# Kernel tuning notes

Measured on AMD Instinct MI355X. Metric: run time of the kernel, lower is better.

Reference implementation:

```python
import jax, jax.numpy as jnp
import numpy as np

EPS = 1e-5

def _layernorm(h, g, b):
    m = jnp.mean(h, axis=-1, keepdims=True)
    v = jnp.mean((h - m) ** 2, axis=-1, keepdims=True)
    return (h - m) * jax.lax.rsqrt(v + EPS) * g + b

def setup_inputs() -> dict:
    key = jax.random.key(0)
    ks = jax.random.split(key, 12)
    B, C, T = 8, 512, 8192
    TOK, CD = 256, 768
    s = 0.02
    return {
        "x": jax.random.normal(ks[0], (B, C, T), dtype=jnp.float32),
        "context": jax.random.normal(ks[1], (B, TOK, CD), dtype=jnp.float32),
        "context_mask": jax.random.randint(ks[2], (B, TOK), 0, 2).astype(bool),
        "ln_g": jnp.ones((C,), jnp.float32),
        "ln_b": jnp.zeros((C,), jnp.float32),
        "cln_g": jnp.ones((CD,), jnp.float32),
        "cln_b": jnp.zeros((CD,), jnp.float32),
        "Wq": jax.random.normal(ks[3], (C, C), jnp.float32) * s,
        "bq": jnp.zeros((C,), jnp.float32),
        "Wk": jax.random.normal(ks[4], (C, CD), jnp.float32) * s,
        "bk": jnp.zeros((C,), jnp.float32),
        "Wv": jax.random.normal(ks[5], (C, CD), jnp.float32) * s,
        "bv": jnp.zeros((C,), jnp.float32),
    }

def reference(x, context, context_mask, ln_g, ln_b, cln_g, cln_b, Wq, bq, Wk, bk, Wv, bv):
    H = 8
    B, C, T = x.shape
    TOK = context.shape[1]
    D = C // H
    hidden = jnp.swapaxes(x, 1, 2)                     # [B, T, C]
    q = (_layernorm(hidden, ln_g, ln_b) @ Wq.T + bq).reshape(B, T, H, D)
    ctx_n = _layernorm(context, cln_g, cln_b)          # [B, TOK, CD]
    k = (ctx_n @ Wk.T + bk).reshape(B, TOK, H, D)
    v = (ctx_n @ Wv.T + bv).reshape(B, TOK, H, D)
    q = jax.nn.softmax(q, axis=-1)                     # feature map on queries
    m = context_mask[:, :, None, None]
    k = jnp.where(m, k, -jnp.finfo(k.dtype).max)
    v = v * m.astype(v.dtype)
    k = jax.nn.softmax(k, axis=1)                      # softmax over tokens
    attn = jnp.einsum('bnhd,bnhe->bhde', k, v)         # small [B,H,D,D] context matrix
    out = jnp.einsum('bthd,bhde->bthe', q, attn).reshape(B, T, C)
    return x + jnp.swapaxes(out, 1, 2)
```

## Files before the change

kernel.cpp:

```cpp
#include <hip/hip_runtime.h>

#define B_ 8
#define C_ 512
#define T_ 8192
#define TOK_ 256
#define CD_ 768

typedef __attribute__((ext_vector_type(8))) short bf16x8;
typedef __attribute__((ext_vector_type(4))) float f32x4;

__device__ __forceinline__ unsigned short f2bf(float f){
  union { float f; unsigned u; } v; v.f = f;
  return (unsigned short)((v.u + 0x7FFFu + ((v.u >> 16) & 1u)) >> 16);
}

__global__ void pack_wq(const float* __restrict__ Wq, unsigned short* __restrict__ out){
  int slot = blockIdx.x * 256 + threadIdx.x;
  int ln = slot & 63, nt = (slot >> 6) & 31, kk = slot >> 11;
  int n  = nt * 16 + (ln & 15);
  int k0 = kk * 32 + (ln >> 4) * 8;
  bf16x8 v;
  #pragma unroll
  for (int j = 0; j < 8; j++) v[j] = (short)f2bf(Wq[(size_t)n * C_ + k0 + j]);
  *(bf16x8*)&out[(size_t)slot * 8] = v;
}

__global__ void pack_wkv(const float* __restrict__ Wk, const float* __restrict__ Wv,
                         unsigned short* __restrict__ out){
  int slot = blockIdx.x * 256 + threadIdx.x;
  int ln = slot & 63, nt = (slot >> 6) & 7;
  int kkh = slot >> 9;
  int kk = kkh % 24, h = kkh / 24;
  const float* W = (nt < 4) ? Wk : Wv;
  int row = h * 64 + (nt & 3) * 16 + (ln & 15);
  int k0 = kk * 32 + (ln >> 4) * 8;
  bf16x8 v;
  #pragma unroll
  for (int j = 0; j < 8; j++) v[j] = (short)f2bf(W[(size_t)row * CD_ + k0 + j]);
  *(bf16x8*)&out[(size_t)slot * 8] = v;
}

__global__ void ctx_ln(const float* __restrict__ ctx, const float* __restrict__ g,
                       const float* __restrict__ bl, unsigned short* __restrict__ outn){
  int row = blockIdx.x;
  const float* p = ctx + (size_t)row * CD_;
  int tid = threadIdx.x;
  float s1 = 0.f, s2 = 0.f;
  for (int i = tid; i < CD_; i += 256){ float v = p[i]; s1 += v; s2 += v * v; }
  #pragma unroll
  for (int o = 32; o > 0; o >>= 1){ s1 += __shfl_xor(s1, o); s2 += __shfl_xor(s2, o); }
  __shared__ float rs[4][2];
  if ((tid & 63) == 0){ rs[tid >> 6][0] = s1; rs[tid >> 6][1] = s2; }
  __syncthreads();
  s1 = rs[0][0] + rs[1][0] + rs[2][0] + rs[3][0];
  s2 = rs[0][1] + rs[1][1] + rs[2][1] + rs[3][1];
  float m = s1 / (float)CD_;
  float var = s2 / (float)CD_ - m * m;
  float rstd = rsqrtf(var + 1e-5f);
  unsigned short* q = outn + (size_t)row * CD_;
  for (int i = tid; i < CD_; i += 256) q[i] = f2bf((p[i] - m) * rstd * g[i] + bl[i]);
}

__global__ __launch_bounds__(256) void ctx_attn(const unsigned short* __restrict__ ctx_nb,
    const unsigned short* __restrict__ wkv_pk,
    const float* __restrict__ bk, const float* __restrict__ bv,
    const int* __restrict__ mask, unsigned short* __restrict__ apk){
  __shared__ __align__(16) char smem[75776];
  unsigned short* a_st  = (unsigned short*)smem;
  unsigned short* p_lds = (unsigned short*)smem;
  unsigned short* v_lds = (unsigned short*)(smem + 32768);
  unsigned short* al    = (unsigned short*)(smem + 65536);
  float* wred = (float*)(smem + 73728);
  int* msk_l  = (int*)(smem + 74752);

  const int tid = threadIdx.x;
  const int b = blockIdx.x >> 3, h = blockIdx.x & 7;
  msk_l[tid] = mask[b * 256 + tid];

  const unsigned short* cb = ctx_nb + (size_t)b * 256 * CD_;
  const int w = tid >> 6, ln = tid & 63, lc = ln & 15, lk = ln >> 4;

  {
    const bf16x8* src = (const bf16x8*)(cb + (size_t)tid * CD_);
    #pragma unroll
    for (int s = 0; s < 4; s++){
      bf16x8 vv = src[s];
      *(bf16x8*)&a_st[(tid * 32 + s * 8) ^ ((tid & 7) << 3)] = vv;
    }
  }
  const bf16x8* wv_ = (const bf16x8*)wkv_pk;
  const size_t wbase = (size_t)h * 24 * 8 * 64;
  f32x4 acc[4][8];
  #pragma unroll
  for (int i = 0; i < 4; i++)
    #pragma unroll
    for (int j = 0; j < 8; j++) acc[i][j] = (f32x4){0.f,0.f,0.f,0.f};
  bf16x8 bbuf[2][8];
  #pragma unroll
  for (int nt = 0; nt < 8; nt++) bbuf[0][nt] = wv_[wbase + (size_t)(0 * 8 + nt) * 64 + ln];
  __syncthreads();

  for (int kk = 0; kk < 24; kk++){
    int cur = kk & 1;
    if (kk < 23){
      const bf16x8* src = (const bf16x8*)(cb + (size_t)tid * CD_ + (kk + 1) * 32);
      unsigned short* dst = a_st + (cur ^ 1) * 8192;
      #pragma unroll
      for (int s = 0; s < 4; s++){
        bf16x8 vv = src[s];
        *(bf16x8*)&dst[(tid * 32 + s * 8) ^ ((tid & 7) << 3)] = vv;
      }
      #pragma unroll
      for (int nt = 0; nt < 8; nt++)
        bbuf[cur ^ 1][nt] = wv_[wbase + (size_t)((kk + 1) * 8 + nt) * 64 + ln];
    }
    bf16x8 af[4];
    #pragma unroll
    for (int mt = 0; mt < 4; mt++){
      int row = w * 64 + mt * 16 + lc;
      af[mt] = *(const bf16x8*)&a_st[cur * 8192 + ((row * 32 + lk * 8) ^ ((row & 7) << 3))];
    }
    #pragma unroll
    for (int mt = 0; mt < 4; mt++)
      #pragma unroll
      for (int nt = 0; nt < 8; nt++)
        acc[mt][nt] = __builtin_amdgcn_mfma_f32_16x16x32_bf16(af[mt], bbuf[cur][nt], acc[mt][nt], 0, 0, 0);
    __syncthreads();
  }

  float bia[8];
  #pragma unroll
  for (int nt = 0; nt < 8; nt++)
    bia[nt] = (nt < 4) ? bk[h * 64 + nt * 16 + lc] : bv[h * 64 + (nt - 4) * 16 + lc];
  bool mk[4][4];
  #pragma unroll
  for (int mt = 0; mt < 4; mt++)
    #pragma unroll
    for (int r = 0; r < 4; r++)
      mk[mt][r] = msk_l[w * 64 + mt * 16 + lk * 4 + r] != 0;

  float cred[4];
  #pragma unroll
  for (int nt = 0; nt < 4; nt++){
    float mx = -3.402823466e38f;
    #pragma unroll
    for (int mt = 0; mt < 4; mt++)
      #pragma unroll
      for (int r = 0; r < 4; r++)
        if (mk[mt][r]) mx = fmaxf(mx, acc[mt][nt][r] + bia[nt]);
    mx = fmaxf(mx, __shfl_xor(mx, 16));
    mx = fmaxf(mx, __shfl_xor(mx, 32));
    cred[nt] = mx;
  }
  if (lk == 0){
    #pragma unroll
    for (int nt = 0; nt < 4; nt++) wred[w * 64 + nt * 16 + lc] = cred[nt];
  }
  __syncthreads();
  float gmx[4];
  #pragma unroll
  for (int nt = 0; nt < 4; nt++){
    int d = nt * 16 + lc;
    gmx[nt] = fmaxf(fmaxf(wred[d], wred[64 + d]), fmaxf(wred[128 + d], wred[192 + d]));
  }
  __syncthreads();
  #pragma unroll
  for (int nt = 0; nt < 4; nt++){
    float s = 0.f;
    #pragma unroll
    for (int mt = 0; mt < 4; mt++)
      #pragma unroll
      for (int r = 0; r < 4; r++){
        float p = mk[mt][r] ? expf(acc[mt][nt][r] + bia[nt] - gmx[nt]) : 0.f;
        acc[mt][nt][r] = p;
        s += p;
      }
    s += __shfl_xor(s, 16);
    s += __shfl_xor(s, 32);
    cred[nt] = s;
  }
  if (lk == 0){
    #pragma unroll
    for (int nt = 0; nt < 4; nt++) wred[w * 64 + nt * 16 + lc] = cred[nt];
  }
  __syncthreads();
  float ginv[4];
  #pragma unroll
  for (int nt = 0; nt < 4; nt++){
    int d = nt * 16 + lc;
    float s = wred[d] + wred[64 + d] + wred[128 + d] + wred[192 + d];
    ginv[nt] = 1.0f / fmaxf(s, 1e-30f);
  }
  #pragma unroll
  for (int nt = 0; nt < 4; nt++){
    int d = nt * 16 + lc;
    #pragma unroll
    for (int mt = 0; mt < 4; mt++)
      #pragma unroll
      for (int r = 0; r < 4; r++){
        int n = w * 64 + mt * 16 + lk * 4 + r;
        p_lds[(d * 256 + n) ^ ((d & 7) << 3)] = f2bf(acc[mt][nt][r] * ginv[nt]);
      }
  }
  #pragma unroll
  for (int nt = 4; nt < 8; nt++){
    int e = (nt - 4) * 16 + lc;
    #pragma unroll
    for (int mt = 0; mt < 4; mt++)
      #pragma unroll
      for (int r = 0; r < 4; r++){
        int n = w * 64 + mt * 16 + lk * 4 + r;
        float vv = mk[mt][r] ? (acc[mt][nt][r] + bia[nt]) : 0.f;
        v_lds[(e * 256 + n) ^ ((e & 7) << 3)] = f2bf(vv);
      }
  }
  __syncthreads();

  f32x4 acc2[4];
  #pragma unroll
  for (int i = 0; i < 4; i++) acc2[i] = (f32x4){0.f,0.f,0.f,0.f};
  #pragma unroll
  for (int kk = 0; kk < 8; kk++){
    int d = w * 16 + lc;
    bf16x8 pa = *(const bf16x8*)&p_lds[(d * 256 + kk * 32 + lk * 8) ^ ((d & 7) << 3)];
    #pragma unroll
    for (int nt2 = 0; nt2 < 4; nt2++){
      int e = nt2 * 16 + lc;
      bf16x8 vb = *(const bf16x8*)&v_lds[(e * 256 + kk * 32 + lk * 8) ^ ((e & 7) << 3)];
      acc2[nt2] = __builtin_amdgcn_mfma_f32_16x16x32_bf16(pa, vb, acc2[nt2], 0, 0, 0);
    }
  }
  #pragma unroll
  for (int nt2 = 0; nt2 < 4; nt2++)
    #pragma unroll
    for (int r = 0; r < 4; r++)
      al[(w * 16 + lk * 4 + r) * 64 + nt2 * 16 + lc] = f2bf(acc2[nt2][r]);
  __syncthreads();

  #pragma unroll
  for (int s2 = 0; s2 < 2; s2++){
    int slot = s2 * 256 + tid;
    int l2 = slot & 63, nt = (slot >> 6) & 3, kk = slot >> 8;
    int e = nt * 16 + (l2 & 15), d0 = kk * 32 + (l2 >> 4) * 8;
    bf16x8 v;
    #pragma unroll
    for (int j = 0; j < 8; j++) v[j] = (short)al[(d0 + j) * 64 + e];
    *(bf16x8*)&apk[((size_t)(b * 8 + h) * 512 + slot) * 8] = v;
  }
}

__global__ __launch_bounds__(256, 3) void fused_main(const float* __restrict__ x,
    const float* __restrict__ g, const float* __restrict__ bl,
    const unsigned short* __restrict__ wq_pk, const float* __restrict__ bq,
    const unsigned short* __restrict__ attn_pk, float* __restrict__ out){
  __shared__ unsigned short a_lds[32 * 512];
  __shared__ float red[32 * 8 * 2];
  __shared__ float m_l[32], rs_l[32];
  const int tid = threadIdx.x;
  const int b = blockIdx.y;
  const int t0 = blockIdx.x * 32;
  const float* xb = x + (size_t)b * C_ * T_ + t0;

  {
    int t = tid & 31, cg = tid >> 5;
    float s1 = 0.f, s2 = 0.f;
    for (int j = 0; j < 64; j++){
      int c = cg * 64 + j;
      float v = xb[(size_t)c * T_ + t];
      s1 += v; s2 += v * v;
    }
    red[(t * 8 + cg) * 2 + 0] = s1;
    red[(t * 8 + cg) * 2 + 1] = s2;
  }
  __syncthreads();
  if (tid < 32){
    float s1 = 0.f, s2 = 0.f;
    #pragma unroll
    for (int j = 0; j < 8; j++){ s1 += red[(tid*8+j)*2]; s2 += red[(tid*8+j)*2+1]; }
    float m = s1 * (1.0f / 512.0f);
    float var = s2 * (1.0f / 512.0f) - m * m;
    m_l[tid] = m;
    rs_l[tid] = rsqrtf(var + 1e-5f);
  }
  __syncthreads();
  {
    int t = tid & 31, cg = tid >> 5;
    float m = m_l[t], rs = rs_l[t];
    for (int o = 0; o < 8; o++){
      int c0 = cg * 64 + o * 8;
      bf16x8 av;
      #pragma unroll
      for (int j = 0; j < 8; j++){
        int c = c0 + j;
        float v = xb[(size_t)c * T_ + t];
        av[j] = (short)f2bf((v - m) * rs * g[c] + bl[c]);
      }
      *(bf16x8*)&a_lds[(t * 512 + c0) ^ ((t & 7) << 3)] = av;
    }
  }
  __syncthreads();

  const int w = tid >> 6, ln = tid & 63, lc = ln & 15, lk = ln >> 4;
  f32x4 acc[2][8];
  #pragma unroll
  for (int i = 0; i < 2; i++)
    #pragma unroll
    for (int j = 0; j < 8; j++) acc[i][j] = (f32x4){0.f, 0.f, 0.f, 0.f};
  const bf16x8* wqv = (const bf16x8*)wq_pk;
  bf16x8 bbuf[2][8];
  #pragma unroll
  for (int nt = 0; nt < 8; nt++) bbuf[0][nt] = wqv[(size_t)(w * 8 + nt) * 64 + ln];
  #pragma unroll
  for (int kk = 0; kk < 16; kk++){
    int cur = kk & 1, nxt = cur ^ 1;
    if (kk < 15){
      #pragma unroll
      for (int nt = 0; nt < 8; nt++)
        bbuf[nxt][nt] = wqv[(size_t)((kk + 1) * 32 + w * 8 + nt) * 64 + ln];
    }
    bf16x8 af[2];
    #pragma unroll
    for (int mt = 0; mt < 2; mt++){
      int t = mt * 16 + lc;
      af[mt] = *(const bf16x8*)&a_lds[(t * 512 + kk * 32 + lk * 8) ^ ((t & 7) << 3)];
    }
    #pragma unroll
    for (int mt = 0; mt < 2; mt++)
      #pragma unroll
      for (int nt = 0; nt < 8; nt++)
        acc[mt][nt] = __builtin_amdgcn_mfma_f32_16x16x32_bf16(af[mt], bbuf[cur][nt], acc[mt][nt], 0, 0, 0);
  }
  bf16x8 b2[2][2][4];
  const bf16x8* apk = (const bf16x8*)attn_pk;
  #pragma unroll
  for (int hh = 0; hh < 2; hh++)
    #pragma unroll
    for (int k2 = 0; k2 < 2; k2++)
      #pragma unroll
      for (int np = 0; np < 4; np++)
        b2[hh][k2][np] = apk[((size_t)(b * 8 + (2 * w + hh)) * 512 + (k2 * 4 + np) * 64 + ln)];
  float bqv[8];
  #pragma unroll
  for (int nt = 0; nt < 8; nt++) bqv[nt] = bq[w * 128 + nt * 16 + lc];
  #pragma unroll
  for (int mt = 0; mt < 2; mt++)
    #pragma unroll
    for (int r = 0; r < 4; r++)
      #pragma unroll
      for (int h2 = 0; h2 < 2; h2++){
        float v[4];
        #pragma unroll
        for (int j = 0; j < 4; j++) v[j] = acc[mt][h2 * 4 + j][r] + bqv[h2 * 4 + j];
        float mx = fmaxf(fmaxf(v[0], v[1]), fmaxf(v[2], v[3]));
        #pragma unroll
        for (int o = 1; o < 16; o <<= 1) mx = fmaxf(mx, __shfl_xor(mx, o));
        float e[4], s = 0.f;
        #pragma unroll
        for (int j = 0; j < 4; j++){ e[j] = expf(v[j] - mx); s += e[j]; }
        #pragma unroll
        for (int o = 1; o < 16; o <<= 1) s += __shfl_xor(s, o);
        float inv = 1.0f / s;
        #pragma unroll
        for (int j = 0; j < 4; j++) acc[mt][h2 * 4 + j][r] = e[j] * inv;
      }
  __syncthreads();
  #pragma unroll
  for (int mt = 0; mt < 2; mt++)
    #pragma unroll
    for (int r = 0; r < 4; r++){
      int t = mt * 16 + lk * 4 + r;
      #pragma unroll
      for (int nt = 0; nt < 8; nt++){
        int col = w * 128 + nt * 16 + lc;
        a_lds[(t * 512 + col) ^ ((t & 7) << 3)] = f2bf(acc[mt][nt][r]);
      }
    }
  __syncthreads();
  f32x4 acc2[2][2][4];
  #pragma unroll
  for (int i = 0; i < 2; i++)
    #pragma unroll
    for (int j = 0; j < 2; j++)
      #pragma unroll
      for (int k = 0; k < 4; k++) acc2[i][j][k] = (f32x4){0.f, 0.f, 0.f, 0.f};
  #pragma unroll
  for (int k2 = 0; k2 < 2; k2++){
    bf16x8 a2[2][2];
    #pragma unroll
    for (int mt = 0; mt < 2; mt++)
      #pragma unroll
      for (int hh = 0; hh < 2; hh++){
        int t = mt * 16 + lc;
        int col = w * 128 + hh * 64 + k2 * 32 + lk * 8;
        a2[mt][hh] = *(const bf16x8*)&a_lds[(t * 512 + col) ^ ((t & 7) << 3)];
      }
    #pragma unroll
    for (int mt = 0; mt < 2; mt++)
      #pragma unroll
      for (int hh = 0; hh < 2; hh++)
        #pragma unroll
        for (int np = 0; np < 4; np++)
          acc2[mt][hh][np] = __builtin_amdgcn_mfma_f32_16x16x32_bf16(a2[mt][hh], b2[hh][k2][np], acc2[mt][hh][np], 0, 0, 0);
  }
  float* trf = (float*)a_lds;
  const int tt = ln & 31;
  const int rowid = (w << 1) | (ln >> 5);
  #pragma unroll
  for (int hh = 0; hh < 2; hh++){
    __syncthreads();
    #pragma unroll
    for (int np = 0; np < 4; np++)
      #pragma unroll
      for (int mt = 0; mt < 2; mt++)
        #pragma unroll
        for (int r = 0; r < 4; r++){
          int t = mt * 16 + lk * 4 + r;
          int cc = w * 64 + np * 16 + lc;
          trf[(t * 256 + cc) ^ (((t & 7) << 2) | ((t >> 3) & 3))] = acc2[mt][hh][np][r];
        }
    __syncthreads();
    #pragma unroll
    for (int i = 0; i < 32; i++){
      int cc = i * 8 + rowid;
      int c = (cc >> 6) * 128 + hh * 64 + (cc & 63);
      float o = trf[(tt * 256 + cc) ^ (((tt & 7) << 2) | ((tt >> 3) & 3))];
      float xv = xb[(size_t)c * T_ + tt];
      out[((size_t)b * C_ + c) * T_ + t0 + tt] = xv + o;
    }
  }
}

extern "C" void kernel_launch(void* const* d_in, const int* in_sizes, int n_in,
                              void* d_out, int out_size, void* d_ws, size_t ws_size,
                              hipStream_t stream) {
  (void)in_sizes; (void)n_in; (void)out_size; (void)ws_size;
  const float* x     = (const float*)d_in[0];
  const float* ctx   = (const float*)d_in[1];
  const int*   mask  = (const int*)d_in[2];
  const float* ln_g  = (const float*)d_in[3];
  const float* ln_b  = (const float*)d_in[4];
  const float* cln_g = (const float*)d_in[5];
  const float* cln_b = (const float*)d_in[6];
  const float* Wq    = (const float*)d_in[7];
  const float* bq    = (const float*)d_in[8];
  const float* Wk    = (const float*)d_in[9];
  const float* bk    = (const float*)d_in[10];
  const float* Wv    = (const float*)d_in[11];
  const float* bv    = (const float*)d_in[12];
  float* out = (float*)d_out;
  char* wsb = (char*)d_ws;
  unsigned short* ctx_nb = (unsigned short*)wsb;
  unsigned short* wq_pk  = (unsigned short*)(wsb + 3145728);
  unsigned short* wkv_pk = (unsigned short*)(wsb + 3670016);
  unsigned short* apk    = (unsigned short*)(wsb + 5242880);

  pack_wq<<<128, 256, 0, stream>>>(Wq, wq_pk);
  pack_wkv<<<384, 256, 0, stream>>>(Wk, Wv, wkv_pk);
  ctx_ln<<<2048, 256, 0, stream>>>(ctx, cln_g, cln_b, ctx_nb);
  ctx_attn<<<64, 256, 0, stream>>>(ctx_nb, wkv_pk, bk, bv, mask, apk);
  fused_main<<<dim3(T_ / 32, B_), 256, 0, stream>>>(x, ln_g, ln_b, wq_pk, bq, apk, out);
}
```

Baseline: 369.2 us.

## Merge prep kernels, cache x in registers, swap output GEMM operands to skip LDS transpose

Folds the three preprocessing kernels (context layernorm and the two weight packers) into one launch with a block-index dispatch. In fused_main, x is read once during the layernorm statistics pass and kept as packed bf16 in registers instead of being read a second time from global memory. The second GEMM now uses the attention matrix as the A operand, so the result comes out channel-major and is written straight to the output without the LDS transpose and its barriers. ctx_attn also defers its LDS stores until after the MFMAs to overlap the global loads. The trade-offs are that the normalized input is now built from bf16-rounded x, the extra registers may lower occupancy, and the direct output stores may coalesce less well.

After: 356.5 us. 1.04x faster.

```diff
diff --git a/kernel.cpp b/kernel.cpp
--- a/kernel.cpp
+++ b/kernel.cpp
@@ -13,52 +13,56 @@
   union { float f; unsigned u; } v; v.f = f;
   return (unsigned short)((v.u + 0x7FFFu + ((v.u >> 16) & 1u)) >> 16);
 }
-
-__global__ void pack_wq(const float* __restrict__ Wq, unsigned short* __restrict__ out){
-  int slot = blockIdx.x * 256 + threadIdx.x;
-  int ln = slot & 63, nt = (slot >> 6) & 31, kk = slot >> 11;
-  int n  = nt * 16 + (ln & 15);
-  int k0 = kk * 32 + (ln >> 4) * 8;
-  bf16x8 v;
-  #pragma unroll
-  for (int j = 0; j < 8; j++) v[j] = (short)f2bf(Wq[(size_t)n * C_ + k0 + j]);
-  *(bf16x8*)&out[(size_t)slot * 8] = v;
-}
-
-__global__ void pack_wkv(const float* __restrict__ Wk, const float* __restrict__ Wv,
-                         unsigned short* __restrict__ out){
-  int slot = blockIdx.x * 256 + threadIdx.x;
-  int ln = slot & 63, nt = (slot >> 6) & 7;
-  int kkh = slot >> 9;
-  int kk = kkh % 24, h = kkh / 24;
-  const float* W = (nt < 4) ? Wk : Wv;
-  int row = h * 64 + (nt & 3) * 16 + (ln & 15);
-  int k0 = kk * 32 + (ln >> 4) * 8;
-  bf16x8 v;
-  #pragma unroll
-  for (int j = 0; j < 8; j++) v[j] = (short)f2bf(W[(size_t)row * CD_ + k0 + j]);
-  *(bf16x8*)&out[(size_t)slot * 8] = v;
-}
-
-__global__ void ctx_ln(const float* __restrict__ ctx, const float* __restrict__ g,
-                       const float* __restrict__ bl, unsigned short* __restrict__ outn){
-  int row = blockIdx.x;
-  const float* p = ctx + (size_t)row * CD_;
-  int tid = threadIdx.x;
-  float s1 = 0.f, s2 = 0.f;
-  for (int i = tid; i < CD_; i += 256){ float v = p[i]; s1 += v; s2 += v * v; }
-  #pragma unroll
-  for (int o = 32; o > 0; o >>= 1){ s1 += __shfl_xor(s1, o); s2 += __shfl_xor(s2, o); }
+__device__ __forceinline__ float bf2f(unsigned short h){
+  union { unsigned u; float f; } v; v.u = ((unsigned)h) << 16;
+  return v.f;
+}
+
+__global__ __launch_bounds__(256) void prep(const float* __restrict__ ctx,
+    const float* __restrict__ cg_, const float* __restrict__ cb_,
+    const float* __restrict__ Wq, const float* __restrict__ Wk, const float* __restrict__ Wv,
+    unsigned short* __restrict__ ctx_nb, unsigned short* __restrict__ wq_pk,
+    unsigned short* __restrict__ wkv_pk){
   __shared__ float rs[4][2];
-  if ((tid & 63) == 0){ rs[tid >> 6][0] = s1; rs[tid >> 6][1] = s2; }
-  __syncthreads();
-  s1 = rs[0][0] + rs[1][0] + rs[2][0] + rs[3][0];
-  s2 = rs[0][1] + rs[1][1] + rs[2][1] + rs[3][1];
-  float m = s1 / (float)CD_;
-  float var = s2 / (float)CD_ - m * m;
-  float rstd = rsqrtf(var + 1e-5f);
-  unsigned short* q = outn + (size_t)row * CD_;
-  for (int i = tid; i < CD_; i += 256) q[i] = f2bf((p[i] - m) * rstd * g[i] + bl[i]);
+  const int bid = blockIdx.x;
+  const int tid = threadIdx.x;
+  if (bid < 2048){
+    const float* p = ctx + (size_t)bid * CD_;
+    float s1 = 0.f, s2 = 0.f;
+    for (int i = tid; i < CD_; i += 256){ float v = p[i]; s1 += v; s2 += v * v; }
+    #pragma unroll
+    for (int o = 32; o > 0; o >>= 1){ s1 += __shfl_xor(s1, o); s2 += __shfl_xor(s2, o); }
+    if ((tid & 63) == 0){ rs[tid >> 6][0] = s1; rs[tid >> 6][1] = s2; }
+    __syncthreads();
+    s1 = rs[0][0] + rs[1][0] + rs[2][0] + rs[3][0];
+    s2 = rs[0][1] + rs[1][1] + rs[2][1] + rs[3][1];
+    float m = s1 / (float)CD_;
+    float var = s2 / (float)CD_ - m * m;
+    float rstd = rsqrtf(var + 1e-5f);
+    unsigned short* q = ctx_nb + (size_t)bid * CD_;
+    for (int i = tid; i < CD_; i += 256) q[i] = f2bf((p[i] - m) * rstd * cg_[i] + cb_[i]);
+  } else if (bid < 2176){
+    int slot = (bid - 2048) * 256 + tid;
+    int ln = slot & 63, nt = (slot >> 6) & 31, kk = slot >> 11;
+    int n  = nt * 16 + (ln & 15);
+    int k0 = kk * 32 + (ln >> 4) * 8;
+    bf16x8 v;
+    #pragma unroll
+    for (int j = 0; j < 8; j++) v[j] = (short)f2bf(Wq[(size_t)n * C_ + k0 + j]);
+    *(bf16x8*)&wq_pk[(size_t)slot * 8] = v;
+  } else {
+    int slot = (bid - 2176) * 256 + tid;
+    int ln = slot & 63, nt = (slot >> 6) & 7;
+    int kkh = slot >> 9;
+    int kk = kkh % 24, h = kkh / 24;
+    const float* W = (nt < 4) ? Wk : Wv;
+    int row = h * 64 + (nt & 3) * 16 + (ln & 15);
+    int k0 = kk * 32 + (ln >> 4) * 8;
+    bf16x8 v;
+    #pragma unroll
+    for (int j = 0; j < 8; j++) v[j] = (short)f2bf(W[(size_t)row * CD_ + k0 + j]);
+    *(bf16x8*)&wkv_pk[(size_t)slot * 8] = v;
+  }
 }
 
 __global__ __launch_bounds__(256) void ctx_attn(const unsigned short* __restrict__ ctx_nb,
@@ -102,14 +106,11 @@
 
   for (int kk = 0; kk < 24; kk++){
     int cur = kk & 1;
+    bf16x8 nx[4];
     if (kk < 23){
       const bf16x8* src = (const bf16x8*)(cb + (size_t)tid * CD_ + (kk + 1) * 32);
-      unsigned short* dst = a_st + (cur ^ 1) * 8192;
-      #pragma unroll
-      for (int s = 0; s < 4; s++){
-        bf16x8 vv = src[s];
-        *(bf16x8*)&dst[(tid * 32 + s * 8) ^ ((tid & 7) << 3)] = vv;
-      }
+      #pragma unroll
+      for (int s = 0; s < 4; s++) nx[s] = src[s];
       #pragma unroll
       for (int nt = 0; nt < 8; nt++)
         bbuf[cur ^ 1][nt] = wv_[wbase + (size_t)((kk + 1) * 8 + nt) * 64 + ln];
@@ -125,6 +126,12 @@
       #pragma unroll
       for (int nt = 0; nt < 8; nt++)
         acc[mt][nt] = __builtin_amdgcn_mfma_f32_16x16x32_bf16(af[mt], bbuf[cur][nt], acc[mt][nt], 0, 0, 0);
+    if (kk < 23){
+      unsigned short* dst = a_st + (cur ^ 1) * 8192;
+      #pragma unroll
+      for (int s = 0; s < 4; s++)
+        *(bf16x8*)&dst[(tid * 32 + s * 8) ^ ((tid & 7) << 3)] = nx[s];
+    }
     __syncthreads();
   }
 
@@ -260,14 +267,17 @@
   const int b = blockIdx.y;
   const int t0 = blockIdx.x * 32;
   const float* xb = x + (size_t)b * C_ * T_ + t0;
-
+  const int t = tid & 31, cg = tid >> 5;
+
+  unsigned int xr[32];
   {
-    int t = tid & 31, cg = tid >> 5;
     float s1 = 0.f, s2 = 0.f;
-    for (int j = 0; j < 64; j++){
-      int c = cg * 64 + j;
-      float v = xb[(size_t)c * T_ + t];
-      s1 += v; s2 += v * v;
+    #pragma unroll
+    for (int jj = 0; jj < 32; jj++){
+      float v0 = xb[(size_t)(cg * 64 + 2 * jj + 0) * T_ + t];
+      float v1 = xb[(size_t)(cg * 64 + 2 * jj + 1) * T_ + t];
+      s1 += v0 + v1; s2 += v0 * v0 + v1 * v1;
+      xr[jj] = (unsigned)f2bf(v0) | ((unsigned)f2bf(v1) << 16);
     }
     red[(t * 8 + cg) * 2 + 0] = s1;
     red[(t * 8 + cg) * 2 + 1] = s2;
@@ -284,15 +294,16 @@
   }
   __syncthreads();
   {
-    int t = tid & 31, cg = tid >> 5;
     float m = m_l[t], rs = rs_l[t];
+    #pragma unroll
     for (int o = 0; o < 8; o++){
       int c0 = cg * 64 + o * 8;
       bf16x8 av;
       #pragma unroll
       for (int j = 0; j < 8; j++){
+        unsigned u = xr[o * 4 + (j >> 1)];
+        float v = bf2f((unsigned short)((j & 1) ? (u >> 16) : (u & 0xffffu)));
         int c = c0 + j;
-        float v = xb[(size_t)c * T_ + t];
         av[j] = (short)f2bf((v - m) * rs * g[c] + bl[c]);
       }
       *(bf16x8*)&a_lds[(t * 512 + c0) ^ ((t & 7) << 3)] = av;
@@ -321,8 +332,8 @@
     bf16x8 af[2];
     #pragma unroll
     for (int mt = 0; mt < 2; mt++){
-      int t = mt * 16 + lc;
-      af[mt] = *(const bf16x8*)&a_lds[(t * 512 + kk * 32 + lk * 8) ^ ((t & 7) << 3)];
+      int tr = mt * 16 + lc;
+      af[mt] = *(const bf16x8*)&a_lds[(tr * 512 + kk * 32 + lk * 8) ^ ((tr & 7) << 3)];
     }
     #pragma unroll
     for (int mt = 0; mt < 2; mt++)
@@ -368,66 +379,53 @@
   for (int mt = 0; mt < 2; mt++)
     #pragma unroll
     for (int r = 0; r < 4; r++){
-      int t = mt * 16 + lk * 4 + r;
+      int tr = mt * 16 + lk * 4 + r;
       #pragma unroll
       for (int nt = 0; nt < 8; nt++){
         int col = w * 128 + nt * 16 + lc;
-        a_lds[(t * 512 + col) ^ ((t & 7) << 3)] = f2bf(acc[mt][nt][r]);
-      }
-    }
-  __syncthreads();
-  f32x4 acc2[2][2][4];
+        a_lds[(tr * 512 + col) ^ ((tr & 7) << 3)] = f2bf(acc[mt][nt][r]);
+      }
+    }
+  __syncthreads();
+  f32x4 acc2[2][4][2];
   #pragma unroll
   for (int i = 0; i < 2; i++)
     #pragma unroll
-    for (int j = 0; j < 2; j++)
-      #pragma unroll
-      for (int k = 0; k < 4; k++) acc2[i][j][k] = (f32x4){0.f, 0.f, 0.f, 0.f};
+    for (int j = 0; j < 4; j++)
+      #pragma unroll
+      for (int k = 0; k < 2; k++) acc2[i][j][k] = (f32x4){0.f, 0.f, 0.f, 0.f};
   #pragma unroll
   for (int k2 = 0; k2 < 2; k2++){
-    bf16x8 a2[2][2];
-    #pragma unroll
-    for (int mt = 0; mt < 2; mt++)
-      #pragma unroll
-      for (int hh = 0; hh < 2; hh++){
-        int t = mt * 16 + lc;
+    bf16x8 pb[2][2];
+    #pragma unroll
+    for (int hh = 0; hh < 2; hh++)
+      #pragma unroll
+      for (int ntt = 0; ntt < 2; ntt++){
+        int tr = ntt * 16 + lc;
         int col = w * 128 + hh * 64 + k2 * 32 + lk * 8;
-        a2[mt][hh] = *(const bf16x8*)&a_lds[(t * 512 + col) ^ ((t & 7) << 3)];
-      }
-    #pragma unroll
-    for (int mt = 0; mt < 2; mt++)
-      #pragma unroll
-      for (int hh = 0; hh < 2; hh++)
-        #pragma unroll
-        for (int np = 0; np < 4; np++)
-          acc2[mt][hh][np] = __builtin_amdgcn_mfma_f32_16x16x32_bf16(a2[mt][hh], b2[hh][k2][np], acc2[mt][hh][np], 0, 0, 0);
-  }
-  float* trf = (float*)a_lds;
-  const int tt = ln & 31;
-  const int rowid = (w << 1) | (ln >> 5);
-  #pragma unroll
-  for (int hh = 0; hh < 2; hh++){
-    __syncthreads();
-    #pragma unroll
-    for (int np = 0; np < 4; np++)
-      #pragma unroll
-      for (int mt = 0; mt < 2; mt++)
+        pb[hh][ntt] = *(const bf16x8*)&a_lds[(tr * 512 + col) ^ ((tr & 7) << 3)];
+      }
+    #pragma unroll
+    for (int hh = 0; hh < 2; hh++)
+      #pragma unroll
+      for (int mtc = 0; mtc < 4; mtc++)
+        #pragma unroll
+        for (int ntt = 0; ntt < 2; ntt++)
+          acc2[hh][mtc][ntt] = __builtin_amdgcn_mfma_f32_16x16x32_bf16(b2[hh][k2][mtc], pb[hh][ntt], acc2[hh][mtc][ntt], 0, 0, 0);
+  }
+  #pragma unroll
+  for (int hh = 0; hh < 2; hh++)
+    #pragma unroll
+    for (int mtc = 0; mtc < 4; mtc++)
+      #pragma unroll
+      for (int ntt = 0; ntt < 2; ntt++)
         #pragma unroll
         for (int r = 0; r < 4; r++){
-          int t = mt * 16 + lk * 4 + r;
-          int cc = w * 64 + np * 16 + lc;
-          trf[(t * 256 + cc) ^ (((t & 7) << 2) | ((t >> 3) & 3))] = acc2[mt][hh][np][r];
+          int c = w * 128 + hh * 64 + mtc * 16 + lk * 4 + r;
+          int tt2 = ntt * 16 + lc;
+          float xv = xb[(size_t)c * T_ + tt2];
+          out[((size_t)b * C_ + c) * T_ + t0 + tt2] = xv + acc2[hh][mtc][ntt][r];
         }
-    __syncthreads();
-    #pragma unroll
-    for (int i = 0; i < 32; i++){
-      int cc = i * 8 + rowid;
-      int c = (cc >> 6) * 128 + hh * 64 + (cc & 63);
-      float o = trf[(tt * 256 + cc) ^ (((tt & 7) << 2) | ((tt >> 3) & 3))];
-      float xv = xb[(size_t)c * T_ + tt];
-      out[((size_t)b * C_ + c) * T_ + t0 + tt] = xv + o;
-    }
-  }
 }
 
 extern "C" void kernel_launch(void* const* d_in, const int* in_sizes, int n_in,
@@ -454,9 +452,7 @@
   unsigned short* wkv_pk = (unsigned short*)(wsb + 3670016);
   unsigned short* apk    = (unsigned short*)(wsb + 5242880);
 
-  pack_wq<<<128, 256, 0, stream>>>(Wq, wq_pk);
-  pack_wkv<<<384, 256, 0, stream>>>(Wk, Wv, wkv_pk);
-  ctx_ln<<<2048, 256, 0, stream>>>(ctx, cln_g, cln_b, ctx_nb);
+  prep<<<2560, 256, 0, stream>>>(ctx, cln_g, cln_b, Wq, Wk, Wv, ctx_nb, wq_pk, wkv_pk);
   ctx_attn<<<64, 256, 0, stream>>>(ctx_nb, wkv_pk, bk, bv, mask, apk);
   fused_main<<<dim3(T_ / 32, B_), 256, 0, stream>>>(x, ln_g, ln_b, wq_pk, bq, apk, out);
 }
```
